# Kernel tuning notes

Measured on AMD Instinct MI355X. Metric: run time of the kernel, lower is better.

Reference implementation:

```python
import jax, jax.numpy as jnp
import numpy as np

B, C, H, W = 4, 384, 56, 56
K, S = 5, 7


def setup_inputs() -> dict:
    key = jax.random.key(0)
    k1, k2, k3, k4, k5 = jax.random.split(key, 5)
    x = jax.random.normal(k1, (B, C, H, W), dtype=jnp.float32)
    ctx = jax.random.normal(k2, (B, C, H, W), dtype=jnp.float32)
    # 1x1 conv weights stored as (out_ch, in_ch) matrices
    Wq = jax.random.normal(k3, (C // 2, C), dtype=jnp.float32) * (1.0 / np.sqrt(C))
    Wk = jax.random.normal(k4, (C // 2, C), dtype=jnp.float32) * (1.0 / np.sqrt(C))
    Wwd = jax.random.normal(k5, (K * K, S * S), dtype=jnp.float32) * (1.0 / np.sqrt(S * S))
    return {"x": x, "ctx": ctx, "Wq": Wq, "Wk": Wk, "Wwd": Wwd}


def reference(x, ctx, Wq, Wk, Wwd):
    b, c, h, w = x.shape
    kk = K
    # q: 1x1 conv then flatten spatial -> (B, C/2, HW)
    q = jnp.einsum('dc,bchw->bdhw', Wq, x).reshape(b, c // 2, h * w)
    # adaptive avg pool to S x S (H,W multiples of S -> uniform 8x8 bins)
    ctx_p = ctx.reshape(b, c, S, h // S, S, w // S).mean(axis=(3, 5))  # (B,C,S,S)
    kf = jnp.einsum('dc,bcst->bdst', Wk, ctx_p).reshape(b, c // 2, S * S)
    # attention over region centers: (B, HW, S*S)
    A = jax.nn.softmax(jnp.einsum('bdn,bds->bns', q, kf), axis=-1)
    # dynamic per-pixel kernels via 1x1 conv S*S -> k*k: (B, k*k, H, W)
    dyn = jnp.einsum('js,bns->bjn', Wwd, A).reshape(b, kk * kk, h, w)
    # unfold x (im2col with padding k//2) -> (B, C, k*k, H, W)
    pad = kk // 2
    xp = jnp.pad(x, ((0, 0), (0, 0), (pad, pad), (pad, pad)))
    patches = jnp.stack(
        [xp[:, :, i:i + h, j:j + w] for i in range(kk) for j in range(kk)], axis=2
    )
    # per-pixel weighted reduction over the k*k taps
    out = jnp.einsum('bcjhw,bjhw->bchw', patches, dyn)
    return out
```

## Files before the change

### kernel.cpp

```cpp
#include <hip/hip_runtime.h>

#define BB 4
#define CCH 384
#define HH 56
#define WWD 56
#define HW 3136
#define S2 49
#define S2P 52
#define D2 192
#define K2 25
#define NBS 196
#define PX 32
#define XS2 32

__global__ __launch_bounds__(256) void gtpool_k(const float* __restrict__ Wa,
                                                const float* __restrict__ Wb,
                                                const float* __restrict__ ctx,
                                                float* __restrict__ GT,
                                                float* __restrict__ PT) {
    __shared__ float sh[6144];
    int blk = blockIdx.x;
    int t = threadIdx.x;
    if (blk < 576) {
        float* As = sh;
        float* Bs = sh + 3072;
        int bi = blk % 24, bj = blk / 24;
        int tj = t & 15, ti = t >> 4;
#pragma unroll
        for (int k = 0; k < 3; k++) {
            int idx = t + 256 * k;
            int d = idx >> 2, q = idx & 3;
            *(float4*)&As[idx * 4] = *(const float4*)&Wa[(size_t)d * CCH + bi * 16 + 4 * q];
            *(float4*)&Bs[idx * 4] = *(const float4*)&Wb[(size_t)d * CCH + bj * 16 + 4 * q];
        }
        __syncthreads();
        float acc = 0.f;
#pragma unroll 8
        for (int d = 0; d < D2; d++)
            acc += As[d * 16 + ti] * Bs[d * 16 + tj];
        GT[(size_t)(bi * 16 + ti) * CCH + bj * 16 + tj] = acc;
    } else {
        float* part = sh;
        int pb = blk - 576;
        int b  = pb / 84;
        int rem = pb - b * 84;
        int sy = rem / 12;
        int cg = rem - sy * 12;
        int c0 = cg * 32;
        const float* base = ctx + ((size_t)(b * CCH + c0)) * HW + sy * 8 * WWD;
#pragma unroll
        for (int k = 0; k < 14; k++) {
            int g = t + 256 * k;
            int cc = g / 112;
            int r2 = g - cc * 112;
            float4 v = *(const float4*)(base + (size_t)cc * HW + 4 * r2);
            part[g] = (v.x + v.y) + (v.z + v.w);
        }
        __syncthreads();
        if (t < 224) {
            int cc = t / 7, sx = t - cc * 7;
            float sum = 0.f;
#pragma unroll
            for (int r = 0; r < 8; r++) {
                sum += part[cc * 112 + r * 14 + 2 * sx]
                     + part[cc * 112 + r * 14 + 2 * sx + 1];
            }
            int bs = b * S2 + sy * 7 + sx;
            PT[(size_t)(c0 + cc) * NBS + bs] = sum * (1.f / 64.f);
        }
    }
}

__global__ __launch_bounds__(256) void mv2_k(const float* __restrict__ GTt,
                                             const float* __restrict__ PT,
                                             float* __restrict__ M) {
    int t = threadIdx.x;
    int r = blockIdx.x * 2 + (t >> 7);
    int c = t & 127;
    bool has1 = (c < NBS - 128);
    int c1 = has1 ? c + 128 : c;
    const float* g = GTt + (size_t)r * CCH;
    float a0 = 0.f, a1 = 0.f;
#pragma unroll 8
    for (int i = 0; i < CCH; i++) {
        float gv = g[i];
        a0 += gv * PT[(size_t)i * NBS + c];
        a1 += gv * PT[(size_t)i * NBS + c1];
    }
    int b0 = c / S2, s0 = c - b0 * S2;
    M[((size_t)(b0 * CCH + r)) * S2P + s0] = a0;
    if (has1) {
        int bs1 = c + 128;
        int b1 = bs1 / S2, s1 = bs1 - b1 * S2;
        M[((size_t)(b1 * CCH + r)) * S2P + s1] = a1;
    }
    if (c >= 68 && c < 80) {
        int rem = c - 68;
        int bb = rem / 3, sp = 49 + rem % 3;
        M[((size_t)(bb * CCH + r)) * S2P + sp] = 0.f;
    }
}

__global__ __launch_bounds__(512, 2) void attn_k(const float* __restrict__ x,
                                                 const float* __restrict__ M,
                                                 const float* __restrict__ Wwd,
                                                 float* __restrict__ dyn) {
    __shared__ __align__(16) float smem[96 * XS2 + 96 * S2P];
    __shared__ __align__(16) float sc[PX * S2P];
    __shared__ __align__(16) float wl[K2 * S2P];
    float* xs  = smem;
    float* Ms  = smem + 96 * XS2;
    float* red = smem;

    int b  = blockIdx.x / 98;
    int n0 = (blockIdx.x % 98) * PX;
    int t  = threadIdx.x;
    int pxg = t & 7, sg = (t >> 3) & 3, slice = t >> 5;

    float4 acc4[4][4];
#pragma unroll
    for (int k = 0; k < 4; k++)
#pragma unroll
        for (int j = 0; j < 4; j++) acc4[k][j] = make_float4(0.f, 0.f, 0.f, 0.f);

    const float* xb = x + (size_t)b * CCH * HW + n0;
    const float* Mb = M + (size_t)b * CCH * S2P;

#pragma unroll
    for (int k = 0; k < 2; k++) {
        int i = t + 512 * k;
        int j = i / S2P, ss = i - j * S2P;
        wl[i] = (ss < S2) ? Wwd[j * S2 + ss] : 0.f;
    }
    if (t < 276) {
        int i = t + 1024;
        int j = i / S2P, ss = i - j * S2P;
        wl[i] = (ss < S2) ? Wwd[j * S2 + ss] : 0.f;
    }

    int rx0 = t >> 3, qx = t & 7;
    int rx1 = rx0 + 64;
    float4 pxa, pxb, pm0, pm1, pm2;

#define ATTN_LOAD(c0)                                                          \
    {                                                                          \
        pxa = *(const float4*)&xb[(size_t)((c0) + rx0) * HW + 4 * qx];         \
        if (t < 256)                                                           \
            pxb = *(const float4*)&xb[(size_t)((c0) + rx1) * HW + 4 * qx];     \
        const float* srcm = Mb + (size_t)(c0) * S2P;                           \
        pm0 = *(const float4*)&srcm[4 * t];                                    \
        pm1 = *(const float4*)&srcm[4 * (t + 512)];                            \
        if (t < 224) pm2 = *(const float4*)&srcm[4 * (t + 1024)];              \
    }

#define ATTN_WRITE()                                                           \
    {                                                                          \
        *(float4*)&xs[rx0 * XS2 + 4 * qx] = pxa;                               \
        if (t < 256) *(float4*)&xs[rx1 * XS2 + 4 * qx] = pxb;                  \
        *(float4*)&Ms[4 * t] = pm0;                                            \
        *(float4*)&Ms[4 * (t + 512)] = pm1;                                    \
        if (t < 224) *(float4*)&Ms[4 * (t + 1024)] = pm2;                      \
    }

    ATTN_LOAD(0);
    for (int ch = 0; ch < 4; ch++) {
        ATTN_WRITE();
        __syncthreads();
        if (ch < 3) { ATTN_LOAD((ch + 1) * 96); }
        int rbase = 6 * slice;
#pragma unroll
        for (int m = 0; m < 6; m++) {
            int r = rbase + m;
            const float4 xv = *(const float4*)&xs[r * XS2 + 4 * pxg];
#pragma unroll
            for (int k = 0; k < 3; k++) {
                int g = sg + 4 * k;
                const float4 mv = *(const float4*)&Ms[r * S2P + 4 * g];
                acc4[k][0].x += mv.x * xv.x; acc4[k][0].y += mv.x * xv.y;
                acc4[k][0].z += mv.x * xv.z; acc4[k][0].w += mv.x * xv.w;
                acc4[k][1].x += mv.y * xv.x; acc4[k][1].y += mv.y * xv.y;
                acc4[k][1].z += mv.y * xv.z; acc4[k][1].w += mv.y * xv.w;
                acc4[k][2].x += mv.z * xv.x; acc4[k][2].y += mv.z * xv.y;
                acc4[k][2].z += mv.z * xv.z; acc4[k][2].w += mv.z * xv.w;
                acc4[k][3].x += mv.w * xv.x; acc4[k][3].y += mv.w * xv.y;
                acc4[k][3].z += mv.w * xv.z; acc4[k][3].w += mv.w * xv.w;
            }
            if (sg == 0) {
                const float4 mv = *(const float4*)&Ms[r * S2P + 48];
                acc4[3][0].x += mv.x * xv.x; acc4[3][0].y += mv.x * xv.y;
                acc4[3][0].z += mv.x * xv.z; acc4[3][0].w += mv.x * xv.w;
                acc4[3][1].x += mv.y * xv.x; acc4[3][1].y += mv.y * xv.y;
                acc4[3][1].z += mv.y * xv.z; acc4[3][1].w += mv.y * xv.w;
                acc4[3][2].x += mv.z * xv.x; acc4[3][2].y += mv.z * xv.y;
                acc4[3][2].z += mv.z * xv.z; acc4[3][2].w += mv.z * xv.w;
                acc4[3][3].x += mv.w * xv.x; acc4[3][3].y += mv.w * xv.y;
                acc4[3][3].z += mv.w * xv.z; acc4[3][3].w += mv.w * xv.w;
            }
        }
        __syncthreads();
    }

#pragma unroll
    for (int k = 0; k < 4; k++)
#pragma unroll
        for (int j = 0; j < 4; j++) {
            acc4[k][j].x += __shfl_xor(acc4[k][j].x, 32);
            acc4[k][j].y += __shfl_xor(acc4[k][j].y, 32);
            acc4[k][j].z += __shfl_xor(acc4[k][j].z, 32);
            acc4[k][j].w += __shfl_xor(acc4[k][j].w, 32);
        }

    int l = t & 63, wv = t >> 6;
    if (wv < 4 && l < 32) {
        float* rb = red + (size_t)wv * PX * S2P;
#pragma unroll
        for (int k = 0; k < 4; k++) {
            int g = sg + 4 * k;
            if (g < 13) {
                *(float4*)&rb[(4 * pxg + 0) * S2P + 4 * g] =
                    make_float4(acc4[k][0].x, acc4[k][1].x, acc4[k][2].x, acc4[k][3].x);
                *(float4*)&rb[(4 * pxg + 1) * S2P + 4 * g] =
                    make_float4(acc4[k][0].y, acc4[k][1].y, acc4[k][2].y, acc4[k][3].y);
                *(float4*)&rb[(4 * pxg + 2) * S2P + 4 * g] =
                    make_float4(acc4[k][0].z, acc4[k][1].z, acc4[k][2].z, acc4[k][3].z);
                *(float4*)&rb[(4 * pxg + 3) * S2P + 4 * g] =
                    make_float4(acc4[k][0].w, acc4[k][1].w, acc4[k][2].w, acc4[k][3].w);
            }
        }
    }
    __syncthreads();
    if (wv >= 4 && l < 32) {
        float* rb = red + (size_t)(wv - 4) * PX * S2P;
#pragma unroll
        for (int k = 0; k < 4; k++) {
            int g = sg + 4 * k;
            if (g < 13) {
                float4 o0 = *(float4*)&rb[(4 * pxg + 0) * S2P + 4 * g];
                float4 o1 = *(float4*)&rb[(4 * pxg + 1) * S2P + 4 * g];
                float4 o2 = *(float4*)&rb[(4 * pxg + 2) * S2P + 4 * g];
                float4 o3 = *(float4*)&rb[(4 * pxg + 3) * S2P + 4 * g];
                o0.x += acc4[k][0].x; o0.y += acc4[k][1].x; o0.z += acc4[k][2].x; o0.w += acc4[k][3].x;
                o1.x += acc4[k][0].y; o1.y += acc4[k][1].y; o1.z += acc4[k][2].y; o1.w += acc4[k][3].y;
                o2.x += acc4[k][0].z; o2.y += acc4[k][1].z; o2.z += acc4[k][2].z; o2.w += acc4[k][3].z;
                o3.x += acc4[k][0].w; o3.y += acc4[k][1].w; o3.z += acc4[k][2].w; o3.w += acc4[k][3].w;
                *(float4*)&rb[(4 * pxg + 0) * S2P + 4 * g] = o0;
                *(float4*)&rb[(4 * pxg + 1) * S2P + 4 * g] = o1;
                *(float4*)&rb[(4 * pxg + 2) * S2P + 4 * g] = o2;
                *(float4*)&rb[(4 * pxg + 3) * S2P + 4 * g] = o3;
            }
        }
    }
    __syncthreads();

    if (t < 416) {
        int px = t / 13, q = t - px * 13;
        float4 ssum = make_float4(0.f, 0.f, 0.f, 0.f);
#pragma unroll
        for (int w = 0; w < 4; w++) {
            float4 vv = *(float4*)&red[(size_t)(w * PX + px) * S2P + 4 * q];
            ssum.x += vv.x; ssum.y += vv.y; ssum.z += vv.z; ssum.w += vv.w;
        }
        *(float4*)&sc[px * S2P + 4 * q] = ssum;
    }
    __syncthreads();

    if (t < 256) {
        int px = t >> 3, li = t & 7;
        float mx = -3.4e38f;
#pragma unroll
        for (int k = 0; k < 7; k++) { int s = li + 8 * k; if (s < S2) mx = fmaxf(mx, sc[px * S2P + s]); }
        mx = fmaxf(mx, __shfl_xor(mx, 1, 8));
        mx = fmaxf(mx, __shfl_xor(mx, 2, 8));
        mx = fmaxf(mx, __shfl_xor(mx, 4, 8));
        float e[7]; float sum = 0.f;
#pragma unroll
        for (int k = 0; k < 7; k++) {
            int s = li + 8 * k;
            if (s < S2) { e[k] = __expf(sc[px * S2P + s] - mx); sum += e[k]; }
        }
        sum += __shfl_xor(sum, 1, 8);
        sum += __shfl_xor(sum, 2, 8);
        sum += __shfl_xor(sum, 4, 8);
        float inv = 1.f / sum;
#pragma unroll
        for (int k = 0; k < 7; k++) {
            int s = li + 8 * k;
            if (s < S2) sc[px * S2P + s] = e[k] * inv;
        }
    }
    __syncthreads();

    float* dynb = dyn + (size_t)b * K2 * HW + n0;
#pragma unroll
    for (int pass = 0; pass < 2; pass++) {
        int o = t + 512 * pass;
        if (pass == 0 || t < 288) {
            int j = o >> 5, px = o & 31;
            float a = 0.f;
#pragma unroll
            for (int q = 0; q < 13; q++) {
                float4 wv4 = *(float4*)&wl[j * S2P + 4 * q];
                float4 pv  = *(float4*)&sc[px * S2P + 4 * q];
                a += wv4.x * pv.x + wv4.y * pv.y + wv4.z * pv.z + wv4.w * pv.w;
            }
            dynb[(size_t)j * HW + px] = a;
        }
    }
#undef ATTN_LOAD
#undef ATTN_WRITE
}

__global__ __launch_bounds__(256, 4) void out_k(const float* __restrict__ x,
                                                const float* __restrict__ dyn,
                                                float* __restrict__ out) {
    __shared__ float xt[8][12][60];
    int blk    = blockIdx.x;
    int cg     = blk % 48;
    int stripe = (blk / 48) % 7;
    int b      = blk / 336;
    int h0 = stripe * 8;
    int c0 = cg * 8;
    int t  = threadIdx.x;
    const float* xb = x + ((size_t)(b * CCH + c0)) * HW;

    if (t < 96) {
        int cc = t / 12, r = t % 12;
        xt[cc][r][0] = 0.f; xt[cc][r][1] = 0.f;
        xt[cc][r][58] = 0.f; xt[cc][r][59] = 0.f;
    }
#pragma unroll
    for (int k = 0; k < 6; k++) {
        int idx = t + 256 * k;
        if (k < 5 || t < 64) {
            int cc  = idx / 168;
            int rem = idx - cc * 168;
            int r   = rem / 14;
            int q   = rem - r * 14;
            int h   = h0 - 2 + r;
            float4 v = make_float4(0.f, 0.f, 0.f, 0.f);
            if ((unsigned)h < (unsigned)HH)
                v = *(const float4*)&xb[(size_t)cc * HW + h * WWD + 4 * q];
            xt[cc][r][2 + 4 * q + 0] = v.x;
            xt[cc][r][2 + 4 * q + 1] = v.y;
            xt[cc][r][2 + 4 * q + 2] = v.z;
            xt[cc][r][2 + 4 * q + 3] = v.w;
        }
    }

    bool act = t < 224;
    int w = t % 56;
    int u = t / 56;
    int n = (h0 + 2 * u) * WWD + w;
    float dv0[K2], dv1[K2];
    if (act) {
        const float* db = dyn + (size_t)b * K2 * HW + n;
#pragma unroll
        for (int j = 0; j < K2; j++) {
            dv0[j] = db[(size_t)j * HW];
            dv1[j] = db[(size_t)j * HW + WWD];
        }
    }
    __syncthreads();
    if (!act) return;

    float* ob = out + ((size_t)(b * CCH + c0)) * HW + n;
#pragma unroll
    for (int cc = 0; cc < 8; cc++) {
        float a0 = 0.f, a1 = 0.f;
#pragma unroll
        for (int rr = 0; rr < 6; rr++) {
            int lr = 2 * u + rr;
            float v0 = xt[cc][lr][w + 0];
            float v1 = xt[cc][lr][w + 1];
            float v2 = xt[cc][lr][w + 2];
            float v3 = xt[cc][lr][w + 3];
            float v4 = xt[cc][lr][w + 4];
            if (rr < 5) {
                int o5 = rr * 5;
                a0 += v0 * dv0[o5] + v1 * dv0[o5 + 1] + v2 * dv0[o5 + 2]
                    + v3 * dv0[o5 + 3] + v4 * dv0[o5 + 4];
            }
            if (rr >= 1) {
                int o5 = (rr - 1) * 5;
                a1 += v0 * dv1[o5] + v1 * dv1[o5 + 1] + v2 * dv1[o5 + 2]
                    + v3 * dv1[o5 + 3] + v4 * dv1[o5 + 4];
            }
        }
        ob[(size_t)cc * HW] = a0;
        ob[(size_t)cc * HW + WWD] = a1;
    }
}

extern "C" void kernel_launch(void* const* d_in, const int* in_sizes, int n_in,
                              void* d_out, int out_size, void* d_ws, size_t ws_size,
                              hipStream_t stream) {
    const float* x   = (const float*)d_in[0];
    const float* ctx = (const float*)d_in[1];
    const float* Wq  = (const float*)d_in[2];
    const float* Wk  = (const float*)d_in[3];
    const float* Wwd = (const float*)d_in[4];
    float* out = (float*)d_out;
    float* ws  = (float*)d_ws;

    float* GT  = ws;
    float* M   = ws + 147456;
    float* dyn = ws + 147456 + 79872;
    float* PT  = dyn;

    gtpool_k<<<576 + 336, 256, 0, stream>>>(Wq, Wk, ctx, GT, PT);
    mv2_k<<<CCH / 2, 256, 0, stream>>>(GT, PT, M);
    attn_k<<<BB * 98, 512, 0, stream>>>(x, M, Wwd, dyn);
    out_k<<<BB * 48 * 7, 256, 0, stream>>>(x, dyn, out);
}
```

Measured before the change: 142.7 us.

## Reorder gtpool blocks, widen mv2 grid, defer Wwd staging, raise out_k occupancy

Several unrelated tweaks land together. The fused gtpool kernel now schedules the memory-bound pooling blocks before the GEMM blocks. mv2 uses one row per block with 196 active threads and four independent accumulators, which doubles the grid and shortens dependency chains. attn_k issues its first x/M prefetch before staging Wwd into shared memory so the global loads overlap. out_k's launch bounds rise from 4 to 5 blocks per SM, which may force register spills.

```diff
diff --git a/kernel.cpp b/kernel.cpp
--- a/kernel.cpp
+++ b/kernel.cpp
@@ -21,10 +21,11 @@
     __shared__ float sh[6144];
     int blk = blockIdx.x;
     int t = threadIdx.x;
-    if (blk < 576) {
+    if (blk >= 336) {
+        int g = blk - 336;
         float* As = sh;
         float* Bs = sh + 3072;
-        int bi = blk % 24, bj = blk / 24;
+        int bi = g % 24, bj = g / 24;
         int tj = t & 15, ti = t >> 4;
 #pragma unroll
         for (int k = 0; k < 3; k++) {
@@ -41,7 +42,7 @@
         GT[(size_t)(bi * 16 + ti) * CCH + bj * 16 + tj] = acc;
     } else {
         float* part = sh;
-        int pb = blk - 576;
+        int pb = blk;
         int b  = pb / 84;
         int rem = pb - b * 84;
         int sy = rem / 12;
@@ -75,27 +76,21 @@
                                              const float* __restrict__ PT,
                                              float* __restrict__ M) {
     int t = threadIdx.x;
-    int r = blockIdx.x * 2 + (t >> 7);
-    int c = t & 127;
-    bool has1 = (c < NBS - 128);
-    int c1 = has1 ? c + 128 : c;
+    int r = blockIdx.x;
     const float* g = GTt + (size_t)r * CCH;
-    float a0 = 0.f, a1 = 0.f;
+    if (t < NBS) {
+        float a0 = 0.f, a1 = 0.f, a2 = 0.f, a3 = 0.f;
 #pragma unroll 8
-    for (int i = 0; i < CCH; i++) {
-        float gv = g[i];
-        a0 += gv * PT[(size_t)i * NBS + c];
-        a1 += gv * PT[(size_t)i * NBS + c1];
-    }
-    int b0 = c / S2, s0 = c - b0 * S2;
-    M[((size_t)(b0 * CCH + r)) * S2P + s0] = a0;
-    if (has1) {
-        int bs1 = c + 128;
-        int b1 = bs1 / S2, s1 = bs1 - b1 * S2;
-        M[((size_t)(b1 * CCH + r)) * S2P + s1] = a1;
-    }
-    if (c >= 68 && c < 80) {
-        int rem = c - 68;
+        for (int i = 0; i < CCH; i += 4) {
+            a0 += g[i + 0] * PT[(size_t)(i + 0) * NBS + t];
+            a1 += g[i + 1] * PT[(size_t)(i + 1) * NBS + t];
+            a2 += g[i + 2] * PT[(size_t)(i + 2) * NBS + t];
+            a3 += g[i + 3] * PT[(size_t)(i + 3) * NBS + t];
+        }
+        int b0 = t / S2, s0 = t - b0 * S2;
+        M[((size_t)(b0 * CCH + r)) * S2P + s0] = (a0 + a1) + (a2 + a3);
+    } else if (t < 208) {
+        int rem = t - 196;
         int bb = rem / 3, sp = 49 + rem % 3;
         M[((size_t)(bb * CCH + r)) * S2P + sp] = 0.f;
     }
@@ -126,18 +121,6 @@
     const float* xb = x + (size_t)b * CCH * HW + n0;
     const float* Mb = M + (size_t)b * CCH * S2P;
 
-#pragma unroll
-    for (int k = 0; k < 2; k++) {
-        int i = t + 512 * k;
-        int j = i / S2P, ss = i - j * S2P;
-        wl[i] = (ss < S2) ? Wwd[j * S2 + ss] : 0.f;
-    }
-    if (t < 276) {
-        int i = t + 1024;
-        int j = i / S2P, ss = i - j * S2P;
-        wl[i] = (ss < S2) ? Wwd[j * S2 + ss] : 0.f;
-    }
-
     int rx0 = t >> 3, qx = t & 7;
     int rx1 = rx0 + 64;
     float4 pxa, pxb, pm0, pm1, pm2;
@@ -163,6 +146,19 @@
     }
 
     ATTN_LOAD(0);
+
+#pragma unroll
+    for (int k = 0; k < 2; k++) {
+        int i = t + 512 * k;
+        int j = i / S2P, ss = i - j * S2P;
+        wl[i] = (ss < S2) ? Wwd[j * S2 + ss] : 0.f;
+    }
+    if (t < 276) {
+        int i = t + 1024;
+        int j = i / S2P, ss = i - j * S2P;
+        wl[i] = (ss < S2) ? Wwd[j * S2 + ss] : 0.f;
+    }
+
     for (int ch = 0; ch < 4; ch++) {
         ATTN_WRITE();
         __syncthreads();
@@ -310,7 +306,7 @@
 #undef ATTN_WRITE
 }
 
-__global__ __launch_bounds__(256, 4) void out_k(const float* __restrict__ x,
+__global__ __launch_bounds__(256, 5) void out_k(const float* __restrict__ x,
                                                 const float* __restrict__ dyn,
                                                 float* __restrict__ out) {
     __shared__ float xt[8][12][60];
@@ -407,8 +403,8 @@
     float* dyn = ws + 147456 + 79872;
     float* PT  = dyn;
 
-    gtpool_k<<<576 + 336, 256, 0, stream>>>(Wq, Wk, ctx, GT, PT);
-    mv2_k<<<CCH / 2, 256, 0, stream>>>(GT, PT, M);
+    gtpool_k<<<336 + 576, 256, 0, stream>>>(Wq, Wk, ctx, GT, PT);
+    mv2_k<<<CCH, 256, 0, stream>>>(GT, PT, M);
     attn_k<<<BB * 98, 512, 0, stream>>>(x, M, Wwd, dyn);
     out_k<<<BB * 48 * 7, 256, 0, stream>>>(x, dyn, out);
 }
```

Result: faster. 135.6 us (-5.0%).
